# Performance work log

Measured on AMD Instinct MI355X. Metric: run time of the kernel, lower is better.

## Reference

```python
import jax, jax.numpy as jnp
import numpy as np
from jax import lax

N = 100000
G = 256          # voxel grid extent per axis
MULT = 8
C_HID = 32 * MULT  # 256
K3 = 27


def setup_inputs() -> dict:
    key = jax.random.key(0)
    k_feat, k1, k2, k3, k4 = jax.random.split(key, 5)
    # unique voxel coordinates in a G^3 grid (sparse tensors have no duplicate coords)
    rng = np.random.default_rng(0)
    lin = rng.choice(G * G * G, size=N, replace=False)
    coords = np.stack([lin // (G * G), (lin // G) % G, lin % G], axis=1).astype(np.int32)
    feats = jax.random.normal(k_feat, (N, 2), dtype=jnp.float32)
    def w(k, cin, cout):
        return jax.random.normal(k, (K3, cin, cout), dtype=jnp.float32) / np.sqrt(K3 * cin)
    return {
        "coords": jnp.asarray(coords),
        "feats": feats,
        "W1": w(k1, 2, C_HID),
        "W2": w(k2, C_HID, C_HID),
        "W3": w(k3, C_HID, C_HID),
        "W4": w(k4, C_HID, 2),
    }


def _neighbor_map(coords):
    """Kernel map for a 3x3x3 stride-1 sparse conv: for each of 27 offsets and each
    point i, the index j of the point at coords[i]+offset (and a validity mask).
    Built once and shared by all four layers (stride=1 preserves coordinates)."""
    S = G + 2  # pad linearization base so offsets in {-1,0,1} never wrap
    c = coords.astype(jnp.int32) + 1
    keys = (c[:, 0] * S + c[:, 1]) * S + c[:, 2]            # [N]
    order = jnp.argsort(keys)
    skeys = keys[order]
    offs = jnp.array([[dx, dy, dz] for dx in (-1, 0, 1)
                      for dy in (-1, 0, 1) for dz in (-1, 0, 1)], dtype=jnp.int32)  # [27,3]
    nc = c[None, :, :] + offs[:, None, :]                    # [27,N,3]
    qk = (nc[..., 0] * S + nc[..., 1]) * S + nc[..., 2]      # [27,N]
    pos = jnp.clip(jnp.searchsorted(skeys, qk), 0, N - 1)
    valid = skeys[pos] == qk                                 # [27,N]
    idx = order[pos]                                         # [27,N]
    return idx, valid


def _sparse_conv(feats, W, idx, valid):
    """gather -> GEMM -> accumulate, scanned over the 27 kernel offsets."""
    out0 = jnp.zeros((feats.shape[0], W.shape[-1]), feats.dtype)
    def step(acc, kv):
        i, v, w = kv
        g = jnp.where(v[:, None], feats[i], 0.0)   # [N,Cin] gathered neighbor feats
        return acc + g @ w, None
    out, _ = lax.scan(step, out0, (idx, valid, W))
    return out


def reference(coords, feats, W1, W2, W3, W4):
    idx, valid = _neighbor_map(coords)
    x = _sparse_conv(feats, W1, idx, valid)
    x = _sparse_conv(x, W2, idx, valid)
    x = _sparse_conv(x, W3, idx, valid)
    x = _sparse_conv(x, W4, idx, valid)
    return x
```

## Files before the change

kernel.cpp:

```cpp
#include <hip/hip_runtime.h>

#define HASH_BITS 19
#define HASH_SIZE (1u << HASH_BITS)
#define HASH_MASK (HASH_SIZE - 1)
#define CH 256
#define PCH 32
#define NREP 8
#define NSEG (27 * NREP)
#define SEGCAP 4096
#define BM_WORDS 536704
#define GD1 4096
#define GH  391
#define GD4 2048
#define GS4 512

typedef __attribute__((ext_vector_type(8))) short short8;
typedef __attribute__((ext_vector_type(4))) float floatx4;
typedef unsigned long long ull;

__device__ __forceinline__ unsigned cvt_pk_bf16(float a, float b) {
    unsigned r;
    asm("v_cvt_pk_bf16_f32 %0, %1, %2" : "=v"(r) : "v"(a), "v"(b));
    return r;
}

__device__ inline void split8_pack(const float* xa, uint4& hv, uint4& lv) {
#pragma unroll
    for (int p = 0; p < 4; ++p) {
        unsigned hp = cvt_pk_bf16(xa[2 * p], xa[2 * p + 1]);
        float h0 = __uint_as_float(hp << 16);
        float h1 = __uint_as_float(hp & 0xFFFF0000u);
        unsigned lp = cvt_pk_bf16(xa[2 * p] - h0, xa[2 * p + 1] - h1);
        ((unsigned*)&hv)[p] = hp;
        ((unsigned*)&lv)[p] = lv.x * 0 + lp;
    }
}

__device__ inline void split8_pack2(const float* xa, uint4& hv, uint4& lv) {
    unsigned hp[4], lp[4];
#pragma unroll
    for (int p = 0; p < 4; ++p) {
        hp[p] = cvt_pk_bf16(xa[2 * p], xa[2 * p + 1]);
        float h0 = __uint_as_float(hp[p] << 16);
        float h1 = __uint_as_float(hp[p] & 0xFFFF0000u);
        lp[p] = cvt_pk_bf16(xa[2 * p] - h0, xa[2 * p + 1] - h1);
    }
    hv.x = hp[0]; hv.y = hp[1]; hv.z = hp[2]; hv.w = hp[3];
    lv.x = lp[0]; lv.y = lp[1]; lv.z = lp[2]; lv.w = lp[3];
}

__global__ void front_fused_k(const int* __restrict__ coords, int n, int gh,
                              ull* __restrict__ tbl, unsigned* __restrict__ keys,
                              unsigned* __restrict__ bm,
                              const float* __restrict__ feats, const float* __restrict__ W1c,
                              float* __restrict__ x1,
                              const float* __restrict__ W2, const float* __restrict__ W3,
                              unsigned short* __restrict__ Whi2, unsigned short* __restrict__ Wlo2,
                              unsigned short* __restrict__ Whi3, unsigned short* __restrict__ Wlo3) {
    int b = blockIdx.x;
    int t = threadIdx.x;
    if (b < GD1) {
        float w0 = W1c[t], w1 = W1c[CH + t];
        for (int i = b; i < n; i += GD1) {
            float2 xv = *reinterpret_cast<const float2*>(feats + 2 * i);
            x1[(size_t)i * CH + t] = fmaf(xv.x, w0, xv.y * w1);
        }
        return;
    }
    b -= GD1;
    if (b < gh) {
        int i = b * 256 + t;
        if (i >= n) return;
        unsigned cx = (unsigned)(coords[3 * i + 0] + 1);
        unsigned cy = (unsigned)(coords[3 * i + 1] + 1);
        unsigned cz = (unsigned)(coords[3 * i + 2] + 1);
        unsigned key = (cx * 258u + cy) * 258u + cz;
        keys[i] = key;
        atomicOr(&bm[key >> 5], 1u << (key & 31));
        ull e = ((ull)key << 32) | (unsigned)i;
        unsigned h = (key * 2654435761u) & HASH_MASK;
        while (true) {
            ull prev = atomicCAS(&tbl[h], 0ull, e);
            if (prev == 0ull) return;
            h = (h + 1) & HASH_MASK;
        }
    }
    b -= gh;
    {
        int tt0 = b * 256 + t;
        const int HALF = 27 * 8 * 256;
        if (tt0 >= 2 * HALF) return;
        const float* W = (tt0 < HALF) ? W2 : W3;
        unsigned short* Whi = (tt0 < HALF) ? Whi2 : Whi3;
        unsigned short* Wlo = (tt0 < HALF) ? Wlo2 : Wlo3;
        int tt = (tt0 < HALF) ? tt0 : tt0 - HALF;
        int cout = tt & 255, kk = (tt >> 8) & 7, k = tt >> 11;
        int nt = cout >> 4, lc = cout & 15;
        const float* src = W + (size_t)k * 65536 + (size_t)kk * 32 * 256 + cout;
        size_t dbase = (((size_t)(k * 8 + kk) * 16 + nt) * 64 + lc) * 8;
#pragma unroll
        for (int kg = 0; kg < 4; ++kg) {
            float xa[8];
#pragma unroll
            for (int j = 0; j < 8; ++j) xa[j] = src[(size_t)(kg * 8 + j) * 256];
            uint4 hv, lv;
            split8_pack2(xa, hv, lv);
            *(uint4*)(Whi + dbase + (size_t)kg * 16 * 8) = hv;
            *(uint4*)(Wlo + dbase + (size_t)kg * 16 * 8) = lv;
        }
    }
}

__global__ void neighbor_bm_k(const unsigned* __restrict__ keys, int n,
                              const unsigned* __restrict__ bm,
                              const ull* __restrict__ tbl,
                              int2* __restrict__ buckets, int* __restrict__ kcnt) {
    int t = blockIdx.x * blockDim.x + threadIdx.x;
    if (t >= n * 9) return;
    int rep = blockIdx.x & (NREP - 1);
    int i = t / 9, r = t - i * 9;
    unsigned key = keys[i];
    int base = (int)key + ((r / 3 - 1) * 258 + (r % 3 - 1)) * 258;
    unsigned bA = base - 1, bB = base, bC = base + 1;
    unsigned hit0 = (bm[bA >> 5] >> (bA & 31)) & 1u;
    unsigned hit1 = (bm[bB >> 5] >> (bB & 31)) & 1u;
    unsigned hit2 = (bm[bC >> 5] >> (bC & 31)) & 1u;
#pragma unroll
    for (int dz = -1; dz <= 1; ++dz) {
        if (r == 4 && dz == 0) continue;
        unsigned hit = dz < 0 ? hit0 : (dz == 0 ? hit1 : hit2);
        if (!hit) continue;
        unsigned nk = (unsigned)(base + dz);
        unsigned h = (nk * 2654435761u) & HASH_MASK;
        int j = -1;
        while (true) {
            ull e = tbl[h];
            if ((unsigned)(e >> 32) == nk) { j = (int)(e & 0xFFFFFFFFu); break; }
            if (e == 0ull) break;
            h = (h + 1) & HASH_MASK;
        }
        if (j >= 0) {
            int kk = 3 * r + dz + 1;
            int seg = kk * NREP + rep;
            int pos = atomicAdd(&kcnt[seg * 16], 1);
            buckets[(size_t)seg * SEGCAP + pos] = make_int2(i, j);
        }
    }
}

__global__ void chunk_desc_k(const int* __restrict__ kcnt,
                             int2* __restrict__ desc, int* __restrict__ nchunks) {
    __shared__ int cnts[NSEG];
    __shared__ int offs[NSEG + 1];
    int t = threadIdx.x;
    if (t < NSEG) cnts[t] = kcnt[t * 16];
    __syncthreads();
    if (t == 0) {
        int acc = 0;
        for (int s = 0; s < NSEG; ++s) { offs[s] = acc; acc += (cnts[s] + PCH - 1) / PCH; }
        offs[NSEG] = acc;
        *nchunks = acc;
    }
    __syncthreads();
    if (t < NSEG) {
        int cnt = cnts[t];
        int o = offs[t];
        int k = t / NREP;
        for (int c = 0; c * PCH < cnt; ++c) {
            int len = min(PCH, cnt - c * PCH);
            desc[o + c] = make_int2(t * SEGCAP + c * PCH, (k << 8) | len);
        }
    }
}

__global__ void sparse1b_k(const float* __restrict__ feats, const float* __restrict__ W1,
                           float* __restrict__ out, const int2* __restrict__ buckets,
                           const int2* __restrict__ desc, const int* __restrict__ nchunks) {
    __shared__ float xs[PCH][2];
    __shared__ int ii[PCH];
    int nc = *nchunks;
    int t = threadIdx.x;
    for (int m = blockIdx.x; m < nc; m += gridDim.x) {
        int2 d = desc[m];
        int k = d.y >> 8, len = d.y & 255;
        if (t < PCH) {
            if (t < len) {
                int2 pr = buckets[d.x + t];
                ii[t] = pr.x;
                xs[t][0] = feats[2 * pr.y];
                xs[t][1] = feats[2 * pr.y + 1];
            } else {
                ii[t] = -1;
                xs[t][0] = 0.f; xs[t][1] = 0.f;
            }
        }
        __syncthreads();
        const float* Wk = W1 + (size_t)k * 2 * CH;
        float w0 = Wk[t], w1 = Wk[CH + t];
#pragma unroll
        for (int p = 0; p < PCH; ++p) {
            int i = ii[p];
            if (i >= 0) atomicAdd(&out[(size_t)i * CH + t], fmaf(xs[p][0], w0, xs[p][1] * w1));
        }
        __syncthreads();
    }
}

__global__ __launch_bounds__(256, 3) void dense_mid_mfma_k(
        const float* __restrict__ x,
        const unsigned short* __restrict__ Whi,
        const unsigned short* __restrict__ Wlo,
        float* __restrict__ out, int n) {
    __shared__ unsigned short AsH[3][2048], AsL[3][2048];
    int t = threadIdx.x;
    int wid = t >> 6, lane = t & 63;
    int i0 = blockIdx.x * 64;

    floatx4 acc[4][4];
#pragma unroll
    for (int a = 0; a < 4; ++a)
#pragma unroll
        for (int b = 0; b < 4; ++b) acc[a][b] = floatx4{0.f, 0.f, 0.f, 0.f};

    int row = ((t >> 6) << 4) + (t & 15);
    int kg = (t >> 4) & 3;
    float sok = (i0 + row < n) ? 1.f : 0.f;
    const float* sp = x + (size_t)min(i0 + row, n - 1) * CH + kg * 8;

    floatx4 ra0, ra1;
    short8 Bh[2][4], Bl[2][4];

    auto loadB = [&](int kk, int b) {
#pragma unroll
        for (int q = 0; q < 4; ++q) {
            size_t off = (((size_t)kk * 16 + wid * 4 + q) * 64 + lane) * 8;
            Bh[b][q] = *(const short8*)&Whi[off];
            Bl[b][q] = *(const short8*)&Wlo[off];
        }
    };
    auto loadA = [&](int kk) {
        ra0 = *(const floatx4*)(sp + kk * 32);
        ra1 = *(const floatx4*)(sp + kk * 32 + 4);
    };
    auto writeA = [&](int bi) {
        float xa[8];
        xa[0] = ra0.x * sok; xa[1] = ra0.y * sok; xa[2] = ra0.z * sok; xa[3] = ra0.w * sok;
        xa[4] = ra1.x * sok; xa[5] = ra1.y * sok; xa[6] = ra1.z * sok; xa[7] = ra1.w * sok;
        uint4 hv, lv;
        split8_pack2(xa, hv, lv);
        *(uint4*)&AsH[bi][t * 8] = hv;
        *(uint4*)&AsL[bi][t * 8] = lv;
    };
    auto compute = [&](int bi, int b) {
#pragma unroll
        for (int mt = 0; mt < 4; ++mt) {
            short8 ah = *(const short8*)&AsH[bi][(mt * 64 + lane) * 8];
            short8 al = *(const short8*)&AsL[bi][(mt * 64 + lane) * 8];
#pragma unroll
            for (int q = 0; q < 4; ++q) {
                acc[mt][q] = __builtin_amdgcn_mfma_f32_16x16x32_bf16(ah, Bh[b][q], acc[mt][q], 0, 0, 0);
                acc[mt][q] = __builtin_amdgcn_mfma_f32_16x16x32_bf16(al, Bh[b][q], acc[mt][q], 0, 0, 0);
                acc[mt][q] = __builtin_amdgcn_mfma_f32_16x16x32_bf16(ah, Bl[b][q], acc[mt][q], 0, 0, 0);
            }
        }
    };

    loadB(0, 0);
    loadA(0); writeA(0);
    loadA(1); writeA(1);
    __syncthreads();

#pragma unroll
    for (int kk = 0; kk < 8; ++kk) {
        if (kk < 7) loadB(kk + 1, (kk + 1) & 1);
        if (kk < 6) loadA(kk + 2);
        compute(kk % 3, kk & 1);
        if (kk < 6) writeA((kk + 2) % 3);
        __syncthreads();
    }

    int r0 = (lane >> 4) * 4, c0 = lane & 15;
#pragma unroll
    for (int mt = 0; mt < 4; ++mt)
#pragma unroll
        for (int r = 0; r < 4; ++r) {
            int orow = i0 + mt * 16 + r0 + r;
            if (orow < n) {
#pragma unroll
                for (int q = 0; q < 4; ++q)
                    out[(size_t)orow * CH + wid * 64 + q * 16 + c0] = acc[mt][q][r];
            }
        }
}

__global__ __launch_bounds__(256) void sparse_mid_mfma_k(
        const float* __restrict__ x,
        const unsigned short* __restrict__ Whi,
        const unsigned short* __restrict__ Wlo,
        float* __restrict__ out, const int2* __restrict__ buckets,
        const int2* __restrict__ desc, const int* __restrict__ nchunks) {
    __shared__ unsigned short As_hi[8192];
    __shared__ unsigned short As_lo[8192];
    __shared__ int ii[PCH];
    int nc = *nchunks;
    int t = threadIdx.x;
    int wid = t >> 6, lane = t & 63;
    int r = t >> 3, kk0 = t & 7;
    int mt_s = r >> 4, rl = r & 15;
    for (int m = blockIdx.x; m < nc; m += gridDim.x) {
        int2 d = desc[m];
        int k = d.y >> 8, len = d.y & 255;
        if (r < len) {
            int2 pr = buckets[d.x + r];
            if (kk0 == 0) ii[r] = pr.x;
            const float* src = x + (size_t)pr.y * CH + kk0 * 32;
#pragma unroll
            for (int kg = 0; kg < 4; ++kg) {
                float xa[8];
                floatx4 v0 = *(const floatx4*)(src + kg * 8);
                floatx4 v1 = *(const floatx4*)(src + kg * 8 + 4);
                xa[0] = v0.x; xa[1] = v0.y; xa[2] = v0.z; xa[3] = v0.w;
                xa[4] = v1.x; xa[5] = v1.y; xa[6] = v1.z; xa[7] = v1.w;
                uint4 hv, lv;
                split8_pack2(xa, hv, lv);
                int ab = ((kk0 * 2 + mt_s) * 64 + kg * 16 + rl) * 8;
                *(uint4*)&As_hi[ab] = hv;
                *(uint4*)&As_lo[ab] = lv;
            }
        } else {
            if (kk0 == 0) ii[r] = -1;
            uint4 z = {0, 0, 0, 0};
#pragma unroll
            for (int kg = 0; kg < 4; ++kg) {
                int ab = ((kk0 * 2 + mt_s) * 64 + kg * 16 + rl) * 8;
                *(uint4*)&As_hi[ab] = z;
                *(uint4*)&As_lo[ab] = z;
            }
        }
        __syncthreads();
        floatx4 acc[2][4];
#pragma unroll
        for (int a = 0; a < 2; ++a)
#pragma unroll
            for (int b = 0; b < 4; ++b) acc[a][b] = floatx4{0.f, 0.f, 0.f, 0.f};

        short8 bh[2][4], bl[2][4];
        auto loadBs = [&](int kk, int b) {
#pragma unroll
            for (int q = 0; q < 4; ++q) {
                size_t off = (((size_t)(k * 8 + kk) * 16 + wid * 4 + q) * 64 + lane) * 8;
                bh[b][q] = *(const short8*)&Whi[off];
                bl[b][q] = *(const short8*)&Wlo[off];
            }
        };
        loadBs(0, 0);
#pragma unroll
        for (int kk = 0; kk < 8; ++kk) {
            if (kk < 7) loadBs(kk + 1, (kk + 1) & 1);
            int b = kk & 1;
            short8 ah0 = *(const short8*)&As_hi[((kk * 2 + 0) * 64 + lane) * 8];
            short8 al0 = *(const short8*)&As_lo[((kk * 2 + 0) * 64 + lane) * 8];
            short8 ah1 = *(const short8*)&As_hi[((kk * 2 + 1) * 64 + lane) * 8];
            short8 al1 = *(const short8*)&As_lo[((kk * 2 + 1) * 64 + lane) * 8];
#pragma unroll
            for (int q = 0; q < 4; ++q) {
                acc[0][q] = __builtin_amdgcn_mfma_f32_16x16x32_bf16(ah0, bh[b][q], acc[0][q], 0, 0, 0);
                acc[0][q] = __builtin_amdgcn_mfma_f32_16x16x32_bf16(al0, bh[b][q], acc[0][q], 0, 0, 0);
                acc[0][q] = __builtin_amdgcn_mfma_f32_16x16x32_bf16(ah0, bl[b][q], acc[0][q], 0, 0, 0);
                acc[1][q] = __builtin_amdgcn_mfma_f32_16x16x32_bf16(ah1, bh[b][q], acc[1][q], 0, 0, 0);
                acc[1][q] = __builtin_amdgcn_mfma_f32_16x16x32_bf16(al1, bh[b][q], acc[1][q], 0, 0, 0);
                acc[1][q] = __builtin_amdgcn_mfma_f32_16x16x32_bf16(ah1, bl[b][q], acc[1][q], 0, 0, 0);
            }
        }
        int r0 = (lane >> 4) * 4, c0 = lane & 15;
#pragma unroll
        for (int mt = 0; mt < 2; ++mt)
#pragma unroll
            for (int rr = 0; rr < 4; ++rr) {
                int orow = mt * 16 + r0 + rr;
                int i = ii[orow];
                if (i >= 0) {
#pragma unroll
                    for (int q = 0; q < 4; ++q)
                        atomicAdd(&out[(size_t)i * CH + wid * 64 + q * 16 + c0], acc[mt][q][rr]);
                }
            }
        __syncthreads();
    }
}

__device__ inline float wave_sum(float v) {
    for (int off = 32; off; off >>= 1) v += __shfl_xor(v, off);
    return v;
}

__global__ void back_fused_k(const float* __restrict__ x, const float* __restrict__ W4,
                             float* __restrict__ out, int n,
                             const int2* __restrict__ buckets,
                             const int2* __restrict__ desc, const int* __restrict__ nchunks) {
    int b = blockIdx.x;
    int wid = threadIdx.x >> 6, lane = threadIdx.x & 63;
    if (b < GD4) {
        const float* Wc = W4 + 13 * CH * 2;
        floatx4 w0 = *reinterpret_cast<const floatx4*>(Wc + lane * 8);
        floatx4 w1 = *reinterpret_cast<const floatx4*>(Wc + lane * 8 + 4);
        for (int i = b * 4 + wid; i < n; i += GD4 * 4) {
            floatx4 xv = *reinterpret_cast<const floatx4*>(x + (size_t)i * CH + lane * 4);
            float a0 = xv.x * w0.x + xv.y * w0.z + xv.z * w1.x + xv.w * w1.z;
            float a1 = xv.x * w0.y + xv.y * w0.w + xv.z * w1.y + xv.w * w1.w;
            a0 = wave_sum(a0);
            a1 = wave_sum(a1);
            if (lane == 0) {
                atomicAdd(&out[2 * i], a0);
                atomicAdd(&out[2 * i + 1], a1);
            }
        }
        return;
    }
    b -= GD4;
    int nc = *nchunks;
    for (int m = b; m < nc; m += GS4) {
        int2 d = desc[m];
        int k = d.y >> 8, len = d.y & 255;
        const float* Wk = W4 + (size_t)k * CH * 2;
        floatx4 w0 = *reinterpret_cast<const floatx4*>(Wk + lane * 8);
        floatx4 w1 = *reinterpret_cast<const floatx4*>(Wk + lane * 8 + 4);
        for (int p = wid; p < len; p += 4) {
            int2 pr = buckets[d.x + p];
            floatx4 xv = *reinterpret_cast<const floatx4*>(x + (size_t)pr.y * CH + lane * 4);
            float a0 = xv.x * w0.x + xv.y * w0.z + xv.z * w1.x + xv.w * w1.z;
            float a1 = xv.x * w0.y + xv.y * w0.w + xv.z * w1.y + xv.w * w1.w;
            a0 = wave_sum(a0);
            a1 = wave_sum(a1);
            if (lane == 0) {
                atomicAdd(&out[2 * pr.x], a0);
                atomicAdd(&out[2 * pr.x + 1], a1);
            }
        }
    }
}

extern "C" void kernel_launch(void* const* d_in, const int* in_sizes, int n_in,
                              void* d_out, int out_size, void* d_ws, size_t ws_size,
                              hipStream_t stream) {
    const int* coords = (const int*)d_in[0];
    const float* feats = (const float*)d_in[1];
    const float* W1 = (const float*)d_in[2];
    const float* W2 = (const float*)d_in[3];
    const float* W3 = (const float*)d_in[4];
    const float* W4 = (const float*)d_in[5];
    float* out = (float*)d_out;
    int n = in_sizes[0] / 3;

    char* ws = (char*)d_ws;
    auto alloc = [&](size_t bytes) -> void* {
        void* p = (void*)ws;
        ws += (bytes + 255) & ~(size_t)255;
        return p;
    };
    ull* tbl = (ull*)alloc((size_t)HASH_SIZE * 8);
    unsigned* bm = (unsigned*)alloc((size_t)BM_WORDS * 4);
    int* kcnt = (int*)alloc((size_t)NSEG * 16 * 4);
    unsigned* keys = (unsigned*)alloc((size_t)n * 4);
    int* nchunks = (int*)alloc(4);
    int ndesc = NSEG * (SEGCAP / PCH);
    int2* desc = (int2*)alloc(sizeof(int2) * (size_t)ndesc);
    int2* buckets = (int2*)alloc(sizeof(int2) * (size_t)NSEG * SEGCAP);
    unsigned short* Whi2 = (unsigned short*)alloc((size_t)27 * 65536 * 2);
    unsigned short* Wlo2 = (unsigned short*)alloc((size_t)27 * 65536 * 2);
    unsigned short* Whi3 = (unsigned short*)alloc((size_t)27 * 65536 * 2);
    unsigned short* Wlo3 = (unsigned short*)alloc((size_t)27 * 65536 * 2);
    float* x1 = (float*)alloc((size_t)n * CH * 4);
    float* x2 = (float*)alloc((size_t)n * CH * 4);

    size_t zspan = (size_t)HASH_SIZE * 8 + (size_t)BM_WORDS * 4 + (size_t)NSEG * 16 * 4;
    hipMemsetAsync(tbl, 0, zspan, stream);
    hipMemsetAsync(out, 0, (size_t)out_size * 4, stream);

    int gh = (n + 255) / 256;
    int gp = (2 * 27 * 8 * 256) / 256;
    front_fused_k<<<GD1 + gh + gp, 256, 0, stream>>>(
        coords, n, gh, tbl, keys, bm,
        feats, W1 + 13 * 2 * CH, x1,
        W2, W3, Whi2, Wlo2, Whi3, Wlo3);

    neighbor_bm_k<<<(n * 9 + 255) / 256, 256, 0, stream>>>(keys, n, bm, tbl, buckets, kcnt);
    chunk_desc_k<<<1, 256, 0, stream>>>(kcnt, desc, nchunks);
    sparse1b_k<<<1024, 256, 0, stream>>>(feats, W1, x1, buckets, desc, nchunks);

    int mtiles = (n + 63) / 64;

    dense_mid_mfma_k<<<mtiles, 256, 0, stream>>>(x1, Whi2 + (size_t)13 * 65536,
                                                 Wlo2 + (size_t)13 * 65536, x2, n);
    sparse_mid_mfma_k<<<512, 256, 0, stream>>>(x1, Whi2, Wlo2, x2, buckets, desc, nchunks);

    dense_mid_mfma_k<<<mtiles, 256, 0, stream>>>(x2, Whi3 + (size_t)13 * 65536,
                                                 Wlo3 + (size_t)13 * 65536, x1, n);
    sparse_mid_mfma_k<<<512, 256, 0, stream>>>(x2, Whi3, Wlo3, x1, buckets, desc, nchunks);

    back_fused_k<<<GD4 + GS4, 256, 0, stream>>>(x1, W4, out, n, buckets, desc, nchunks);
}
```

Measured before the change: 252.6 us.

## Drop chunk-descriptor kernel and map blocks directly to segment chunks

Removes the single-block chunk_desc kernel and the desc/nchunks arrays. The sparse kernels now launch a fixed grid of NSEG*NCHK blocks, where each block reads its segment count from kcnt and exits early if its chunk is empty. The neighbor search is moved into the kernel that also does the layer-1 centre GEMV and the weight splitting, so it overlaps with that work. Hash insertion becomes its own kernel that runs first. This cuts one launch and one serial dependency step. The cost is many idle blocks, and each segment is assumed to hold at most NCHK*PCH pairs, which the sparse inputs satisfy.

```diff
diff --git a/kernel.cpp b/kernel.cpp
--- a/kernel.cpp
+++ b/kernel.cpp
@@ -8,11 +8,10 @@
 #define NREP 8
 #define NSEG (27 * NREP)
 #define SEGCAP 4096
+#define NCHK 16
 #define BM_WORDS 536704
 #define GD1 4096
-#define GH  391
 #define GD4 2048
-#define GS4 512
 
 typedef __attribute__((ext_vector_type(8))) short short8;
 typedef __attribute__((ext_vector_type(4))) float floatx4;
@@ -22,18 +21,6 @@
     unsigned r;
     asm("v_cvt_pk_bf16_f32 %0, %1, %2" : "=v"(r) : "v"(a), "v"(b));
     return r;
-}
-
-__device__ inline void split8_pack(const float* xa, uint4& hv, uint4& lv) {
-#pragma unroll
-    for (int p = 0; p < 4; ++p) {
-        unsigned hp = cvt_pk_bf16(xa[2 * p], xa[2 * p + 1]);
-        float h0 = __uint_as_float(hp << 16);
-        float h1 = __uint_as_float(hp & 0xFFFF0000u);
-        unsigned lp = cvt_pk_bf16(xa[2 * p] - h0, xa[2 * p + 1] - h1);
-        ((unsigned*)&hv)[p] = hp;
-        ((unsigned*)&lv)[p] = lv.x * 0 + lp;
-    }
 }
 
 __device__ inline void split8_pack2(const float* xa, uint4& hv, uint4& lv) {
@@ -49,45 +36,82 @@
     lv.x = lp[0]; lv.y = lp[1]; lv.z = lp[2]; lv.w = lp[3];
 }
 
-__global__ void front_fused_k(const int* __restrict__ coords, int n, int gh,
+__global__ void hash_insert_k(const int* __restrict__ coords, int n,
                               ull* __restrict__ tbl, unsigned* __restrict__ keys,
-                              unsigned* __restrict__ bm,
-                              const float* __restrict__ feats, const float* __restrict__ W1c,
-                              float* __restrict__ x1,
-                              const float* __restrict__ W2, const float* __restrict__ W3,
-                              unsigned short* __restrict__ Whi2, unsigned short* __restrict__ Wlo2,
-                              unsigned short* __restrict__ Whi3, unsigned short* __restrict__ Wlo3) {
+                              unsigned* __restrict__ bm) {
+    int i = blockIdx.x * blockDim.x + threadIdx.x;
+    if (i >= n) return;
+    unsigned cx = (unsigned)(coords[3 * i + 0] + 1);
+    unsigned cy = (unsigned)(coords[3 * i + 1] + 1);
+    unsigned cz = (unsigned)(coords[3 * i + 2] + 1);
+    unsigned key = (cx * 258u + cy) * 258u + cz;
+    keys[i] = key;
+    atomicOr(&bm[key >> 5], 1u << (key & 31));
+    ull e = ((ull)key << 32) | (unsigned)i;
+    unsigned h = (key * 2654435761u) & HASH_MASK;
+    while (true) {
+        ull prev = atomicCAS(&tbl[h], 0ull, e);
+        if (prev == 0ull) return;
+        h = (h + 1) & HASH_MASK;
+    }
+}
+
+__global__ void stage2_k(const unsigned* __restrict__ keys, int n, int gnb,
+                         const unsigned* __restrict__ bm, const ull* __restrict__ tbl,
+                         int2* __restrict__ buckets, int* __restrict__ kcnt,
+                         const float* __restrict__ feats, const float* __restrict__ W1c,
+                         float* __restrict__ x1,
+                         const float* __restrict__ W2, const float* __restrict__ W3,
+                         unsigned short* __restrict__ Whi2, unsigned short* __restrict__ Wlo2,
+                         unsigned short* __restrict__ Whi3, unsigned short* __restrict__ Wlo3) {
     int b = blockIdx.x;
-    int t = threadIdx.x;
+    int tid = threadIdx.x;
+    if (b < gnb) {
+        int t = b * 256 + tid;
+        if (t >= n * 9) return;
+        int rep = b & (NREP - 1);
+        int i = t / 9, r = t - i * 9;
+        unsigned key = keys[i];
+        int base = (int)key + ((r / 3 - 1) * 258 + (r % 3 - 1)) * 258;
+        unsigned bA = base - 1, bB = base, bC = base + 1;
+        unsigned hit0 = (bm[bA >> 5] >> (bA & 31)) & 1u;
+        unsigned hit1 = (bm[bB >> 5] >> (bB & 31)) & 1u;
+        unsigned hit2 = (bm[bC >> 5] >> (bC & 31)) & 1u;
+#pragma unroll
+        for (int dz = -1; dz <= 1; ++dz) {
+            if (r == 4 && dz == 0) continue;
+            unsigned hit = dz < 0 ? hit0 : (dz == 0 ? hit1 : hit2);
+            if (!hit) continue;
+            unsigned nk = (unsigned)(base + dz);
+            unsigned h = (nk * 2654435761u) & HASH_MASK;
+            int j = -1;
+            while (true) {
+                ull e = tbl[h];
+                if ((unsigned)(e >> 32) == nk) { j = (int)(e & 0xFFFFFFFFu); break; }
+                if (e == 0ull) break;
+                h = (h + 1) & HASH_MASK;
+            }
+            if (j >= 0) {
+                int kk = 3 * r + dz + 1;
+                int seg = kk * NREP + rep;
+                int pos = atomicAdd(&kcnt[seg * 16], 1);
+                buckets[(size_t)seg * SEGCAP + pos] = make_int2(i, j);
+            }
+        }
+        return;
+    }
+    b -= gnb;
     if (b < GD1) {
-        float w0 = W1c[t], w1 = W1c[CH + t];
+        float w0 = W1c[tid], w1 = W1c[CH + tid];
         for (int i = b; i < n; i += GD1) {
             float2 xv = *reinterpret_cast<const float2*>(feats + 2 * i);
-            x1[(size_t)i * CH + t] = fmaf(xv.x, w0, xv.y * w1);
+            x1[(size_t)i * CH + tid] = fmaf(xv.x, w0, xv.y * w1);
         }
         return;
     }
     b -= GD1;
-    if (b < gh) {
-        int i = b * 256 + t;
-        if (i >= n) return;
-        unsigned cx = (unsigned)(coords[3 * i + 0] + 1);
-        unsigned cy = (unsigned)(coords[3 * i + 1] + 1);
-        unsigned cz = (unsigned)(coords[3 * i + 2] + 1);
-        unsigned key = (cx * 258u + cy) * 258u + cz;
-        keys[i] = key;
-        atomicOr(&bm[key >> 5], 1u << (key & 31));
-        ull e = ((ull)key << 32) | (unsigned)i;
-        unsigned h = (key * 2654435761u) & HASH_MASK;
-        while (true) {
-            ull prev = atomicCAS(&tbl[h], 0ull, e);
-            if (prev == 0ull) return;
-            h = (h + 1) & HASH_MASK;
-        }
-    }
-    b -= gh;
     {
-        int tt0 = b * 256 + t;
+        int tt0 = b * 256 + tid;
         const int HALF = 27 * 8 * 256;
         if (tt0 >= 2 * HALF) return;
         const float* W = (tt0 < HALF) ? W2 : W3;
@@ -111,98 +135,36 @@
     }
 }
 
-__global__ void neighbor_bm_k(const unsigned* __restrict__ keys, int n,
-                              const unsigned* __restrict__ bm,
-                              const ull* __restrict__ tbl,
-                              int2* __restrict__ buckets, int* __restrict__ kcnt) {
-    int t = blockIdx.x * blockDim.x + threadIdx.x;
-    if (t >= n * 9) return;
-    int rep = blockIdx.x & (NREP - 1);
-    int i = t / 9, r = t - i * 9;
-    unsigned key = keys[i];
-    int base = (int)key + ((r / 3 - 1) * 258 + (r % 3 - 1)) * 258;
-    unsigned bA = base - 1, bB = base, bC = base + 1;
-    unsigned hit0 = (bm[bA >> 5] >> (bA & 31)) & 1u;
-    unsigned hit1 = (bm[bB >> 5] >> (bB & 31)) & 1u;
-    unsigned hit2 = (bm[bC >> 5] >> (bC & 31)) & 1u;
-#pragma unroll
-    for (int dz = -1; dz <= 1; ++dz) {
-        if (r == 4 && dz == 0) continue;
-        unsigned hit = dz < 0 ? hit0 : (dz == 0 ? hit1 : hit2);
-        if (!hit) continue;
-        unsigned nk = (unsigned)(base + dz);
-        unsigned h = (nk * 2654435761u) & HASH_MASK;
-        int j = -1;
-        while (true) {
-            ull e = tbl[h];
-            if ((unsigned)(e >> 32) == nk) { j = (int)(e & 0xFFFFFFFFu); break; }
-            if (e == 0ull) break;
-            h = (h + 1) & HASH_MASK;
-        }
-        if (j >= 0) {
-            int kk = 3 * r + dz + 1;
-            int seg = kk * NREP + rep;
-            int pos = atomicAdd(&kcnt[seg * 16], 1);
-            buckets[(size_t)seg * SEGCAP + pos] = make_int2(i, j);
-        }
-    }
-}
-
-__global__ void chunk_desc_k(const int* __restrict__ kcnt,
-                             int2* __restrict__ desc, int* __restrict__ nchunks) {
-    __shared__ int cnts[NSEG];
-    __shared__ int offs[NSEG + 1];
-    int t = threadIdx.x;
-    if (t < NSEG) cnts[t] = kcnt[t * 16];
-    __syncthreads();
-    if (t == 0) {
-        int acc = 0;
-        for (int s = 0; s < NSEG; ++s) { offs[s] = acc; acc += (cnts[s] + PCH - 1) / PCH; }
-        offs[NSEG] = acc;
-        *nchunks = acc;
-    }
-    __syncthreads();
-    if (t < NSEG) {
-        int cnt = cnts[t];
-        int o = offs[t];
-        int k = t / NREP;
-        for (int c = 0; c * PCH < cnt; ++c) {
-            int len = min(PCH, cnt - c * PCH);
-            desc[o + c] = make_int2(t * SEGCAP + c * PCH, (k << 8) | len);
-        }
-    }
-}
-
 __global__ void sparse1b_k(const float* __restrict__ feats, const float* __restrict__ W1,
                            float* __restrict__ out, const int2* __restrict__ buckets,
-                           const int2* __restrict__ desc, const int* __restrict__ nchunks) {
+                           const int* __restrict__ kcnt) {
     __shared__ float xs[PCH][2];
     __shared__ int ii[PCH];
-    int nc = *nchunks;
+    int seg = blockIdx.x / NCHK, c = blockIdx.x % NCHK;
+    int cnt = kcnt[seg * 16];
+    if (c * PCH >= cnt) return;
+    int len = min(PCH, cnt - c * PCH);
+    int k = seg / NREP;
+    int start = seg * SEGCAP + c * PCH;
     int t = threadIdx.x;
-    for (int m = blockIdx.x; m < nc; m += gridDim.x) {
-        int2 d = desc[m];
-        int k = d.y >> 8, len = d.y & 255;
-        if (t < PCH) {
-            if (t < len) {
-                int2 pr = buckets[d.x + t];
-                ii[t] = pr.x;
-                xs[t][0] = feats[2 * pr.y];
-                xs[t][1] = feats[2 * pr.y + 1];
-            } else {
-                ii[t] = -1;
-                xs[t][0] = 0.f; xs[t][1] = 0.f;
-            }
-        }
-        __syncthreads();
-        const float* Wk = W1 + (size_t)k * 2 * CH;
-        float w0 = Wk[t], w1 = Wk[CH + t];
-#pragma unroll
-        for (int p = 0; p < PCH; ++p) {
-            int i = ii[p];
-            if (i >= 0) atomicAdd(&out[(size_t)i * CH + t], fmaf(xs[p][0], w0, xs[p][1] * w1));
-        }
-        __syncthreads();
+    if (t < PCH) {
+        if (t < len) {
+            int2 pr = buckets[start + t];
+            ii[t] = pr.x;
+            xs[t][0] = feats[2 * pr.y];
+            xs[t][1] = feats[2 * pr.y + 1];
+        } else {
+            ii[t] = -1;
+            xs[t][0] = 0.f; xs[t][1] = 0.f;
+        }
+    }
+    __syncthreads();
+    const float* Wk = W1 + (size_t)k * 2 * CH;
+    float w0 = Wk[t], w1 = Wk[CH + t];
+#pragma unroll
+    for (int p = 0; p < PCH; ++p) {
+        int i = ii[p];
+        if (i >= 0) atomicAdd(&out[(size_t)i * CH + t], fmaf(xs[p][0], w0, xs[p][1] * w1));
     }
 }
 
@@ -298,95 +260,95 @@
         const unsigned short* __restrict__ Whi,
         const unsigned short* __restrict__ Wlo,
         float* __restrict__ out, const int2* __restrict__ buckets,
-        const int2* __restrict__ desc, const int* __restrict__ nchunks) {
+        const int* __restrict__ kcnt) {
     __shared__ unsigned short As_hi[8192];
     __shared__ unsigned short As_lo[8192];
     __shared__ int ii[PCH];
-    int nc = *nchunks;
+    int seg = blockIdx.x / NCHK, c = blockIdx.x % NCHK;
+    int cnt = kcnt[seg * 16];
+    if (c * PCH >= cnt) return;
+    int len = min(PCH, cnt - c * PCH);
+    int k = seg / NREP;
+    int start = seg * SEGCAP + c * PCH;
     int t = threadIdx.x;
     int wid = t >> 6, lane = t & 63;
     int r = t >> 3, kk0 = t & 7;
     int mt_s = r >> 4, rl = r & 15;
-    for (int m = blockIdx.x; m < nc; m += gridDim.x) {
-        int2 d = desc[m];
-        int k = d.y >> 8, len = d.y & 255;
-        if (r < len) {
-            int2 pr = buckets[d.x + r];
-            if (kk0 == 0) ii[r] = pr.x;
-            const float* src = x + (size_t)pr.y * CH + kk0 * 32;
-#pragma unroll
-            for (int kg = 0; kg < 4; ++kg) {
-                float xa[8];
-                floatx4 v0 = *(const floatx4*)(src + kg * 8);
-                floatx4 v1 = *(const floatx4*)(src + kg * 8 + 4);
-                xa[0] = v0.x; xa[1] = v0.y; xa[2] = v0.z; xa[3] = v0.w;
-                xa[4] = v1.x; xa[5] = v1.y; xa[6] = v1.z; xa[7] = v1.w;
-                uint4 hv, lv;
-                split8_pack2(xa, hv, lv);
-                int ab = ((kk0 * 2 + mt_s) * 64 + kg * 16 + rl) * 8;
-                *(uint4*)&As_hi[ab] = hv;
-                *(uint4*)&As_lo[ab] = lv;
-            }
-        } else {
-            if (kk0 == 0) ii[r] = -1;
-            uint4 z = {0, 0, 0, 0};
-#pragma unroll
-            for (int kg = 0; kg < 4; ++kg) {
-                int ab = ((kk0 * 2 + mt_s) * 64 + kg * 16 + rl) * 8;
-                *(uint4*)&As_hi[ab] = z;
-                *(uint4*)&As_lo[ab] = z;
-            }
-        }
-        __syncthreads();
-        floatx4 acc[2][4];
-#pragma unroll
-        for (int a = 0; a < 2; ++a)
-#pragma unroll
-            for (int b = 0; b < 4; ++b) acc[a][b] = floatx4{0.f, 0.f, 0.f, 0.f};
-
-        short8 bh[2][4], bl[2][4];
-        auto loadBs = [&](int kk, int b) {
-#pragma unroll
-            for (int q = 0; q < 4; ++q) {
-                size_t off = (((size_t)(k * 8 + kk) * 16 + wid * 4 + q) * 64 + lane) * 8;
-                bh[b][q] = *(const short8*)&Whi[off];
-                bl[b][q] = *(const short8*)&Wlo[off];
-            }
-        };
-        loadBs(0, 0);
-#pragma unroll
-        for (int kk = 0; kk < 8; ++kk) {
-            if (kk < 7) loadBs(kk + 1, (kk + 1) & 1);
-            int b = kk & 1;
-            short8 ah0 = *(const short8*)&As_hi[((kk * 2 + 0) * 64 + lane) * 8];
-            short8 al0 = *(const short8*)&As_lo[((kk * 2 + 0) * 64 + lane) * 8];
-            short8 ah1 = *(const short8*)&As_hi[((kk * 2 + 1) * 64 + lane) * 8];
-            short8 al1 = *(const short8*)&As_lo[((kk * 2 + 1) * 64 + lane) * 8];
-#pragma unroll
-            for (int q = 0; q < 4; ++q) {
-                acc[0][q] = __builtin_amdgcn_mfma_f32_16x16x32_bf16(ah0, bh[b][q], acc[0][q], 0, 0, 0);
-                acc[0][q] = __builtin_amdgcn_mfma_f32_16x16x32_bf16(al0, bh[b][q], acc[0][q], 0, 0, 0);
-                acc[0][q] = __builtin_amdgcn_mfma_f32_16x16x32_bf16(ah0, bl[b][q], acc[0][q], 0, 0, 0);
-                acc[1][q] = __builtin_amdgcn_mfma_f32_16x16x32_bf16(ah1, bh[b][q], acc[1][q], 0, 0, 0);
-                acc[1][q] = __builtin_amdgcn_mfma_f32_16x16x32_bf16(al1, bh[b][q], acc[1][q], 0, 0, 0);
-                acc[1][q] = __builtin_amdgcn_mfma_f32_16x16x32_bf16(ah1, bl[b][q], acc[1][q], 0, 0, 0);
-            }
-        }
-        int r0 = (lane >> 4) * 4, c0 = lane & 15;
-#pragma unroll
-        for (int mt = 0; mt < 2; ++mt)
-#pragma unroll
-            for (int rr = 0; rr < 4; ++rr) {
-                int orow = mt * 16 + r0 + rr;
-                int i = ii[orow];
-                if (i >= 0) {
-#pragma unroll
-                    for (int q = 0; q < 4; ++q)
-                        atomicAdd(&out[(size_t)i * CH + wid * 64 + q * 16 + c0], acc[mt][q][rr]);
-                }
-            }
-        __syncthreads();
-    }
+    if (r < len) {
+        int2 pr = buckets[start + r];
+        if (kk0 == 0) ii[r] = pr.x;
+        const float* src = x + (size_t)pr.y * CH + kk0 * 32;
+#pragma unroll
+        for (int kg = 0; kg < 4; ++kg) {
+            float xa[8];
+            floatx4 v0 = *(const floatx4*)(src + kg * 8);
+            floatx4 v1 = *(const floatx4*)(src + kg * 8 + 4);
+            xa[0] = v0.x; xa[1] = v0.y; xa[2] = v0.z; xa[3] = v0.w;
+            xa[4] = v1.x; xa[5] = v1.y; xa[6] = v1.z; xa[7] = v1.w;
+            uint4 hv, lv;
+            split8_pack2(xa, hv, lv);
+            int ab = ((kk0 * 2 + mt_s) * 64 + kg * 16 + rl) * 8;
+            *(uint4*)&As_hi[ab] = hv;
+            *(uint4*)&As_lo[ab] = lv;
+        }
+    } else {
+        if (kk0 == 0) ii[r] = -1;
+        uint4 z = {0, 0, 0, 0};
+#pragma unroll
+        for (int kg = 0; kg < 4; ++kg) {
+            int ab = ((kk0 * 2 + mt_s) * 64 + kg * 16 + rl) * 8;
+            *(uint4*)&As_hi[ab] = z;
+            *(uint4*)&As_lo[ab] = z;
+        }
+    }
+    __syncthreads();
+    floatx4 acc[2][4];
+#pragma unroll
+    for (int a = 0; a < 2; ++a)
+#pragma unroll
+        for (int b = 0; b < 4; ++b) acc[a][b] = floatx4{0.f, 0.f, 0.f, 0.f};
+
+    short8 bh[2][4], bl[2][4];
+    auto loadBs = [&](int kk, int b) {
+#pragma unroll
+        for (int q = 0; q < 4; ++q) {
+            size_t off = (((size_t)(k * 8 + kk) * 16 + wid * 4 + q) * 64 + lane) * 8;
+            bh[b][q] = *(const short8*)&Whi[off];
+            bl[b][q] = *(const short8*)&Wlo[off];
+        }
+    };
+    loadBs(0, 0);
+#pragma unroll
+    for (int kk = 0; kk < 8; ++kk) {
+        if (kk < 7) loadBs(kk + 1, (kk + 1) & 1);
+        int b = kk & 1;
+        short8 ah0 = *(const short8*)&As_hi[((kk * 2 + 0) * 64 + lane) * 8];
+        short8 al0 = *(const short8*)&As_lo[((kk * 2 + 0) * 64 + lane) * 8];
+        short8 ah1 = *(const short8*)&As_hi[((kk * 2 + 1) * 64 + lane) * 8];
+        short8 al1 = *(const short8*)&As_lo[((kk * 2 + 1) * 64 + lane) * 8];
+#pragma unroll
+        for (int q = 0; q < 4; ++q) {
+            acc[0][q] = __builtin_amdgcn_mfma_f32_16x16x32_bf16(ah0, bh[b][q], acc[0][q], 0, 0, 0);
+            acc[0][q] = __builtin_amdgcn_mfma_f32_16x16x32_bf16(al0, bh[b][q], acc[0][q], 0, 0, 0);
+            acc[0][q] = __builtin_amdgcn_mfma_f32_16x16x32_bf16(ah0, bl[b][q], acc[0][q], 0, 0, 0);
+            acc[1][q] = __builtin_amdgcn_mfma_f32_16x16x32_bf16(ah1, bh[b][q], acc[1][q], 0, 0, 0);
+            acc[1][q] = __builtin_amdgcn_mfma_f32_16x16x32_bf16(al1, bh[b][q], acc[1][q], 0, 0, 0);
+            acc[1][q] = __builtin_amdgcn_mfma_f32_16x16x32_bf16(ah1, bl[b][q], acc[1][q], 0, 0, 0);
+        }
+    }
+    int r0 = (lane >> 4) * 4, c0 = lane & 15;
+#pragma unroll
+    for (int mt = 0; mt < 2; ++mt)
+#pragma unroll
+        for (int rr = 0; rr < 4; ++rr) {
+            int orow = mt * 16 + r0 + rr;
+            int i = ii[orow];
+            if (i >= 0) {
+#pragma unroll
+                for (int q = 0; q < 4; ++q)
+                    atomicAdd(&out[(size_t)i * CH + wid * 64 + q * 16 + c0], acc[mt][q][rr]);
+            }
+        }
 }
 
 __device__ inline float wave_sum(float v) {
@@ -397,7 +359,7 @@
 __global__ void back_fused_k(const float* __restrict__ x, const float* __restrict__ W4,
                              float* __restrict__ out, int n,
                              const int2* __restrict__ buckets,
-                             const int2* __restrict__ desc, const int* __restrict__ nchunks) {
+                             const int* __restrict__ kcnt) {
     int b = blockIdx.x;
     int wid = threadIdx.x >> 6, lane = threadIdx.x & 63;
     if (b < GD4) {
@@ -418,24 +380,25 @@
         return;
     }
     b -= GD4;
-    int nc = *nchunks;
-    for (int m = b; m < nc; m += GS4) {
-        int2 d = desc[m];
-        int k = d.y >> 8, len = d.y & 255;
-        const float* Wk = W4 + (size_t)k * CH * 2;
-        floatx4 w0 = *reinterpret_cast<const floatx4*>(Wk + lane * 8);
-        floatx4 w1 = *reinterpret_cast<const floatx4*>(Wk + lane * 8 + 4);
-        for (int p = wid; p < len; p += 4) {
-            int2 pr = buckets[d.x + p];
-            floatx4 xv = *reinterpret_cast<const floatx4*>(x + (size_t)pr.y * CH + lane * 4);
-            float a0 = xv.x * w0.x + xv.y * w0.z + xv.z * w1.x + xv.w * w1.z;
-            float a1 = xv.x * w0.y + xv.y * w0.w + xv.z * w1.y + xv.w * w1.w;
-            a0 = wave_sum(a0);
-            a1 = wave_sum(a1);
-            if (lane == 0) {
-                atomicAdd(&out[2 * pr.x], a0);
-                atomicAdd(&out[2 * pr.x + 1], a1);
-            }
+    int seg = b / NCHK, c = b % NCHK;
+    int cnt = kcnt[seg * 16];
+    if (c * PCH >= cnt) return;
+    int len = min(PCH, cnt - c * PCH);
+    int k = seg / NREP;
+    int start = seg * SEGCAP + c * PCH;
+    const float* Wk = W4 + (size_t)k * CH * 2;
+    floatx4 w0 = *reinterpret_cast<const floatx4*>(Wk + lane * 8);
+    floatx4 w1 = *reinterpret_cast<const floatx4*>(Wk + lane * 8 + 4);
+    for (int p = wid; p < len; p += 4) {
+        int2 pr = buckets[start + p];
+        floatx4 xv = *reinterpret_cast<const floatx4*>(x + (size_t)pr.y * CH + lane * 4);
+        float a0 = xv.x * w0.x + xv.y * w0.z + xv.z * w1.x + xv.w * w1.z;
+        float a1 = xv.x * w0.y + xv.y * w0.w + xv.z * w1.y + xv.w * w1.w;
+        a0 = wave_sum(a0);
+        a1 = wave_sum(a1);
+        if (lane == 0) {
+            atomicAdd(&out[2 * pr.x], a0);
+            atomicAdd(&out[2 * pr.x + 1], a1);
         }
     }
 }
@@ -462,9 +425,6 @@
     unsigned* bm = (unsigned*)alloc((size_t)BM_WORDS * 4);
     int* kcnt = (int*)alloc((size_t)NSEG * 16 * 4);
     unsigned* keys = (unsigned*)alloc((size_t)n * 4);
-    int* nchunks = (int*)alloc(4);
-    int ndesc = NSEG * (SEGCAP / PCH);
-    int2* desc = (int2*)alloc(sizeof(int2) * (size_t)ndesc);
     int2* buckets = (int2*)alloc(sizeof(int2) * (size_t)NSEG * SEGCAP);
     unsigned short* Whi2 = (unsigned short*)alloc((size_t)27 * 65536 * 2);
     unsigned short* Wlo2 = (unsigned short*)alloc((size_t)27 * 65536 * 2);
@@ -478,25 +438,26 @@
     hipMemsetAsync(out, 0, (size_t)out_size * 4, stream);
 
     int gh = (n + 255) / 256;
+    hash_insert_k<<<gh, 256, 0, stream>>>(coords, n, tbl, keys, bm);
+
+    int gnb = (n * 9 + 255) / 256;
     int gp = (2 * 27 * 8 * 256) / 256;
-    front_fused_k<<<GD1 + gh + gp, 256, 0, stream>>>(
-        coords, n, gh, tbl, keys, bm,
+    stage2_k<<<gnb + GD1 + gp, 256, 0, stream>>>(
+        keys, n, gnb, bm, tbl, buckets, kcnt,
         feats, W1 + 13 * 2 * CH, x1,
         W2, W3, Whi2, Wlo2, Whi3, Wlo3);
 
-    neighbor_bm_k<<<(n * 9 + 255) / 256, 256, 0, stream>>>(keys, n, bm, tbl, buckets, kcnt);
-    chunk_desc_k<<<1, 256, 0, stream>>>(kcnt, desc, nchunks);
-    sparse1b_k<<<1024, 256, 0, stream>>>(feats, W1, x1, buckets, desc, nchunks);
+    sparse1b_k<<<NSEG * NCHK, 256, 0, stream>>>(feats, W1, x1, buckets, kcnt);
 
     int mtiles = (n + 63) / 64;
 
     dense_mid_mfma_k<<<mtiles, 256, 0, stream>>>(x1, Whi2 + (size_t)13 * 65536,
                                                  Wlo2 + (size_t)13 * 65536, x2, n);
-    sparse_mid_mfma_k<<<512, 256, 0, stream>>>(x1, Whi2, Wlo2, x2, buckets, desc, nchunks);
+    sparse_mid_mfma_k<<<NSEG * NCHK, 256, 0, stream>>>(x1, Whi2, Wlo2, x2, buckets, kcnt);
 
     dense_mid_mfma_k<<<mtiles, 256, 0, stream>>>(x2, Whi3 + (size_t)13 * 65536,
                                                  Wlo3 + (size_t)13 * 65536, x1, n);
-    sparse_mid_mfma_k<<<512, 256, 0, stream>>>(x2, Whi3, Wlo3, x1, buckets, desc, nchunks);
-
-    back_fused_k<<<GD4 + GS4, 256, 0, stream>>>(x1, W4, out, n, buckets, desc, nchunks);
-}
+    sparse_mid_mfma_k<<<NSEG * NCHK, 256, 0, stream>>>(x2, Whi3, Wlo3, x1, buckets, kcnt);
+
+    back_fused_k<<<GD4 + NSEG * NCHK, 256, 0, stream>>>(x1, W4, out, n, buckets, kcnt);
+}
```

Result: slower. 322.8 us (+27.8%).

## Double sparse-conv chunk size to 64 rows per block for weight reuse

Applied to the files above, without the earlier changes.

Raises the per-chunk row count in the mid-layer MFMA kernel from 32 to 64, so each block gathers 64 neighbor rows and computes four 16-row M tiles per weight fragment. Each loaded bf16 hi/lo weight fragment is now reused across twice as many rows, cutting weight traffic per output. In exchange LDS use doubles to 64KB and the accumulators grow, which lowers occupancy. Bucket chunks that are less than full also waste more MFMA work on zero-padded rows. It also removes an unused helper and define.

```diff
diff --git a/kernel.cpp b/kernel.cpp
--- a/kernel.cpp
+++ b/kernel.cpp
@@ -4,13 +4,12 @@
 #define HASH_SIZE (1u << HASH_BITS)
 #define HASH_MASK (HASH_SIZE - 1)
 #define CH 256
-#define PCH 32
+#define PCH 64
 #define NREP 8
 #define NSEG (27 * NREP)
 #define SEGCAP 4096
 #define BM_WORDS 536704
 #define GD1 4096
-#define GH  391
 #define GD4 2048
 #define GS4 512
 
@@ -22,18 +21,6 @@
     unsigned r;
     asm("v_cvt_pk_bf16_f32 %0, %1, %2" : "=v"(r) : "v"(a), "v"(b));
     return r;
-}
-
-__device__ inline void split8_pack(const float* xa, uint4& hv, uint4& lv) {
-#pragma unroll
-    for (int p = 0; p < 4; ++p) {
-        unsigned hp = cvt_pk_bf16(xa[2 * p], xa[2 * p + 1]);
-        float h0 = __uint_as_float(hp << 16);
-        float h1 = __uint_as_float(hp & 0xFFFF0000u);
-        unsigned lp = cvt_pk_bf16(xa[2 * p] - h0, xa[2 * p + 1] - h1);
-        ((unsigned*)&hv)[p] = hp;
-        ((unsigned*)&lv)[p] = lv.x * 0 + lp;
-    }
 }
 
 __device__ inline void split8_pack2(const float* xa, uint4& hv, uint4& lv) {
@@ -299,48 +286,57 @@
         const unsigned short* __restrict__ Wlo,
         float* __restrict__ out, const int2* __restrict__ buckets,
         const int2* __restrict__ desc, const int* __restrict__ nchunks) {
-    __shared__ unsigned short As_hi[8192];
-    __shared__ unsigned short As_lo[8192];
+    __shared__ unsigned short As_hi[16384];
+    __shared__ unsigned short As_lo[16384];
     __shared__ int ii[PCH];
     int nc = *nchunks;
     int t = threadIdx.x;
     int wid = t >> 6, lane = t & 63;
-    int r = t >> 3, kk0 = t & 7;
+    int r = t >> 2;
+    int s4 = t & 3;
     int mt_s = r >> 4, rl = r & 15;
     for (int m = blockIdx.x; m < nc; m += gridDim.x) {
         int2 d = desc[m];
         int k = d.y >> 8, len = d.y & 255;
         if (r < len) {
             int2 pr = buckets[d.x + r];
-            if (kk0 == 0) ii[r] = pr.x;
-            const float* src = x + (size_t)pr.y * CH + kk0 * 32;
-#pragma unroll
-            for (int kg = 0; kg < 4; ++kg) {
-                float xa[8];
-                floatx4 v0 = *(const floatx4*)(src + kg * 8);
-                floatx4 v1 = *(const floatx4*)(src + kg * 8 + 4);
-                xa[0] = v0.x; xa[1] = v0.y; xa[2] = v0.z; xa[3] = v0.w;
-                xa[4] = v1.x; xa[5] = v1.y; xa[6] = v1.z; xa[7] = v1.w;
-                uint4 hv, lv;
-                split8_pack2(xa, hv, lv);
-                int ab = ((kk0 * 2 + mt_s) * 64 + kg * 16 + rl) * 8;
-                *(uint4*)&As_hi[ab] = hv;
-                *(uint4*)&As_lo[ab] = lv;
+            if (s4 == 0) ii[r] = pr.x;
+            const float* src = x + (size_t)pr.y * CH;
+#pragma unroll
+            for (int h = 0; h < 2; ++h) {
+                int kk0 = s4 + h * 4;
+#pragma unroll
+                for (int kg = 0; kg < 4; ++kg) {
+                    float xa[8];
+                    floatx4 v0 = *(const floatx4*)(src + kk0 * 32 + kg * 8);
+                    floatx4 v1 = *(const floatx4*)(src + kk0 * 32 + kg * 8 + 4);
+                    xa[0] = v0.x; xa[1] = v0.y; xa[2] = v0.z; xa[3] = v0.w;
+                    xa[4] = v1.x; xa[5] = v1.y; xa[6] = v1.z; xa[7] = v1.w;
+                    uint4 hv, lv;
+                    split8_pack2(xa, hv, lv);
+                    int ab = ((kk0 * 4 + mt_s) * 64 + kg * 16 + rl) * 8;
+                    *(uint4*)&As_hi[ab] = hv;
+                    *(uint4*)&As_lo[ab] = lv;
+                }
             }
         } else {
-            if (kk0 == 0) ii[r] = -1;
+            if (s4 == 0) ii[r] = -1;
             uint4 z = {0, 0, 0, 0};
 #pragma unroll
-            for (int kg = 0; kg < 4; ++kg) {
-                int ab = ((kk0 * 2 + mt_s) * 64 + kg * 16 + rl) * 8;
-                *(uint4*)&As_hi[ab] = z;
-                *(uint4*)&As_lo[ab] = z;
+            for (int h = 0; h < 2; ++h) {
+                int kk0 = s4 + h * 4;
+#pragma unroll
+                for (int kg = 0; kg < 4; ++kg) {
+                    int ab = ((kk0 * 4 + mt_s) * 64 + kg * 16 + rl) * 8;
+                    *(uint4*)&As_hi[ab] = z;
+                    *(uint4*)&As_lo[ab] = z;
+                }
             }
         }
         __syncthreads();
-        floatx4 acc[2][4];
-#pragma unroll
-        for (int a = 0; a < 2; ++a)
+        floatx4 acc[4][4];
+#pragma unroll
+        for (int a = 0; a < 4; ++a)
 #pragma unroll
             for (int b = 0; b < 4; ++b) acc[a][b] = floatx4{0.f, 0.f, 0.f, 0.f};
 
@@ -358,23 +354,21 @@
         for (int kk = 0; kk < 8; ++kk) {
             if (kk < 7) loadBs(kk + 1, (kk + 1) & 1);
             int b = kk & 1;
-            short8 ah0 = *(const short8*)&As_hi[((kk * 2 + 0) * 64 + lane) * 8];
-            short8 al0 = *(const short8*)&As_lo[((kk * 2 + 0) * 64 + lane) * 8];
-            short8 ah1 = *(const short8*)&As_hi[((kk * 2 + 1) * 64 + lane) * 8];
-            short8 al1 = *(const short8*)&As_lo[((kk * 2 + 1) * 64 + lane) * 8];
-#pragma unroll
-            for (int q = 0; q < 4; ++q) {
-                acc[0][q] = __builtin_amdgcn_mfma_f32_16x16x32_bf16(ah0, bh[b][q], acc[0][q], 0, 0, 0);
-                acc[0][q] = __builtin_amdgcn_mfma_f32_16x16x32_bf16(al0, bh[b][q], acc[0][q], 0, 0, 0);
-                acc[0][q] = __builtin_amdgcn_mfma_f32_16x16x32_bf16(ah0, bl[b][q], acc[0][q], 0, 0, 0);
-                acc[1][q] = __builtin_amdgcn_mfma_f32_16x16x32_bf16(ah1, bh[b][q], acc[1][q], 0, 0, 0);
-                acc[1][q] = __builtin_amdgcn_mfma_f32_16x16x32_bf16(al1, bh[b][q], acc[1][q], 0, 0, 0);
-                acc[1][q] = __builtin_amdgcn_mfma_f32_16x16x32_bf16(ah1, bl[b][q], acc[1][q], 0, 0, 0);
+#pragma unroll
+            for (int mt = 0; mt < 4; ++mt) {
+                short8 ah = *(const short8*)&As_hi[((kk * 4 + mt) * 64 + lane) * 8];
+                short8 al = *(const short8*)&As_lo[((kk * 4 + mt) * 64 + lane) * 8];
+#pragma unroll
+                for (int q = 0; q < 4; ++q) {
+                    acc[mt][q] = __builtin_amdgcn_mfma_f32_16x16x32_bf16(ah, bh[b][q], acc[mt][q], 0, 0, 0);
+                    acc[mt][q] = __builtin_amdgcn_mfma_f32_16x16x32_bf16(al, bh[b][q], acc[mt][q], 0, 0, 0);
+                    acc[mt][q] = __builtin_amdgcn_mfma_f32_16x16x32_bf16(ah, bl[b][q], acc[mt][q], 0, 0, 0);
+                }
             }
         }
         int r0 = (lane >> 4) * 4, c0 = lane & 15;
 #pragma unroll
-        for (int mt = 0; mt < 2; ++mt)
+        for (int mt = 0; mt < 4; ++mt)
 #pragma unroll
             for (int rr = 0; rr < 4; ++rr) {
                 int orow = mt * 16 + r0 + rr;
```

Result: no change. 256.2 us (+1.4%).
